# Kernel optimization log

Measured on AMD Instinct MI355X. Metric: run time of the kernel, lower is better.

The kernel has to match this reference:

```python
import jax, jax.numpy as jnp
import numpy as np

NU, NI, E, D, B, L = 100000, 50000, 800000, 64, 1024, 2
P_DROP, TEMP = 0.25, 0.2
L1, L2, L3 = 0.2, 0.01, 1e-5


def setup_inputs() -> dict:
    k = jax.random.split(jax.random.key(0), 20)
    s = 0.02  # xavier-ish scale for embedding tables
    return dict(
        E_u_0=jax.random.normal(k[0], (NU, D), jnp.float32) * s,
        E_i_0=jax.random.normal(k[1], (NI, D), jnp.float32) * s,
        fuse_w=jax.random.normal(k[2], (E,), jnp.float32),
        fuse_b=jax.random.normal(k[3], (E,), jnp.float32),
        W1u=jax.random.normal(k[4], (D, D), jnp.float32) / np.sqrt(D),
        W1i=jax.random.normal(k[5], (D, D), jnp.float32) / np.sqrt(D),
        b1=jnp.zeros((D,), jnp.float32),
        W2=jax.random.normal(k[6], (D,), jnp.float32) / np.sqrt(D),
        b2=jnp.zeros((1,), jnp.float32),
        att_a=jax.random.normal(k[7], (2 * D,), jnp.float32) / np.sqrt(2 * D),
        wv_param=jax.random.normal(k[8], (E,), jnp.float32),
        Wg=jax.random.normal(k[9], (D, D), jnp.float32) / np.sqrt(D),
        adj_vals=jax.random.uniform(k[10], (E,), jnp.float32, 0.001, 0.02),
        drop_main_u=jax.random.uniform(k[11], (2 * L, E), jnp.float32),
        drop_aug_u=jax.random.uniform(k[12], (2 * L, E), jnp.float32),
        edge_src=jax.random.randint(k[13], (E,), 0, NU),
        edge_dst=jax.random.randint(k[14], (E,), 0, NI),
        uids=jax.random.randint(k[15], (B,), 0, NU),
        iids=jax.random.randint(k[16], (B,), 0, NI),
        pos_ids=jax.random.randint(k[17], (B,), 0, NI),
        neg_ids=jax.random.randint(k[18], (B,), 0, NI),
    )


def _forward(E_u_0, E_i_0, fuse_w, fuse_b, W1u, W1i, b1, W2, b2, att_a,
             wv_param, Wg, adj_vals, drop_main_u, drop_aug_u,
             edge_src, edge_dst, uids, iids, pos_ids, neg_ids):
    dt = adj_vals.dtype

    def spmm_u(vals, Xi):  # A @ Xi -> [NU, D]
        return jax.ops.segment_sum(vals[:, None] * Xi[edge_dst], edge_src, num_segments=NU)

    def spmm_i(vals, Xu):  # A.T @ Xu -> [NI, D]
        return jax.ops.segment_sum(vals[:, None] * Xu[edge_src], edge_dst, num_segments=NI)

    def mask(u):  # sparse_dropout: keep w.p. 1-p, rescale
        return (u > P_DROP).astype(dt) / (1.0 - P_DROP)

    def propagate(vals, drops):  # LightGCN-style sum over layers
        Eu, Ei = E_u_0, E_i_0
        Su, Si = Eu, Ei
        for layer in range(L):
            Eu_n = spmm_u(vals * mask(drops[2 * layer]), Ei)
            Ei_n = spmm_i(vals * mask(drops[2 * layer + 1]), Eu)
            Eu, Ei = Eu_n, Ei_n
            Su, Si = Su + Eu, Si + Ei
        return Su, Si

    E_u, E_i = propagate(adj_vals, drop_main_u)

    eu0, ei0 = E_u_0[edge_src], E_i_0[edge_dst]  # [E, D]
    # MLP view
    h = jax.nn.relu(eu0 @ W1u + ei0 @ W1i + b1)
    Ag_mlp = jax.nn.sigmoid(h @ W2 + b2[0])
    # WV view: learnable per-edge weight
    Ag_wv = jax.nn.sigmoid(wv_param)
    # GCN view: one propagation on current embeddings, bilinear edge score
    h_u = spmm_u(adj_vals, E_i)
    h_i = spmm_i(adj_vals, E_u)
    Ag_gcn = jax.nn.sigmoid(jnp.sum((h_u[edge_src] @ Wg) * h_i[edge_dst], axis=1))
    # ATT view: GAT-style
    Ag_att = jax.nn.sigmoid(jax.nn.leaky_relu(eu0 @ att_a[:D] + ei0 @ att_a[D:], 0.2))

    views = jnp.stack([Ag_mlp, Ag_wv, Ag_gcn, Ag_att])  # [4, E]
    w = jax.nn.softmax(jnp.tanh(fuse_w * views + fuse_b), axis=1)  # softmax over edges (as in source)
    Ag = jnp.sum(w * views, axis=0)
    Ag = (Ag + (views - Ag).sum(0)) / 5.0  # mlp_cof = 1 -> (sum(views) - 3*Ag) / 5

    # refine: sigmoid of endpoint dot products
    pre = jax.nn.sigmoid(jnp.sum(E_u[edge_src] * E_i[edge_dst], axis=1))
    baew = pre * Ag  # batch_aug_edge_weight

    aug_vals = jax.lax.stop_gradient(baew) * adj_vals  # new_graph * adj_norm (detach + Hadamard)
    Z_u, Z_i = propagate(aug_vals, drop_aug_u)

    # contrastive loss
    Gu, Gi = Z_u[uids], Z_i[iids]
    neg_sc = jnp.log(jnp.exp(Gu @ E_u.T / TEMP).sum(1) + 1e-8).mean() \
           + jnp.log(jnp.exp(Gi @ E_i.T / TEMP).sum(1) + 1e-8).mean()
    pos_sc = jnp.clip((Gu * E_u[uids]).sum(1) / TEMP, -5.0, 5.0).mean() \
           + jnp.clip((Gi * E_i[iids]).sum(1) / TEMP, -5.0, 5.0).mean()
    loss_cl = -pos_sc + neg_sc

    # BPR loss
    u_e, p_e, n_e = E_u[uids], E_i[pos_ids], E_i[neg_ids]
    diff = (u_e * p_e).sum(-1) - (u_e * n_e).sum(-1)
    loss_bpr = -jnp.log(jax.nn.sigmoid(diff)).mean()

    loss_pr = L2 * (-jnp.log(baew)).mean()

    params = [E_u_0, E_i_0, fuse_w, fuse_b, W1u, W1i, b1, W2, b2, att_a, wv_param, Wg]
    loss_reg = L3 * sum((p_ ** 2).sum() for p_ in params)

    loss = loss_bpr + L1 * loss_cl + loss_pr + loss_reg
    return loss, loss_bpr, L1 * loss_cl, loss_pr


def reference(E_u_0, E_i_0, fuse_w, fuse_b, W1u, W1i, b1, W2, b2, att_a,
              wv_param, Wg, adj_vals, drop_main_u, drop_aug_u,
              edge_src, edge_dst, uids, iids, pos_ids, neg_ids):
    return _forward(E_u_0, E_i_0, fuse_w, fuse_b, W1u, W1i, b1, W2, b2, att_a,
                    wv_param, Wg, adj_vals, drop_main_u, drop_aug_u,
                    edge_src, edge_dst, uids, iids, pos_ids, neg_ids)
```

## Files before the change

kernel.cpp:

```cpp
#include <hip/hip_runtime.h>
#include <math.h>

constexpr int NUc = 100000;
constexpr int NIc = 50000;
constexpr int Ec  = 800000;
constexpr int Bc  = 1024;

typedef __attribute__((ext_vector_type(8))) short short8;
typedef __attribute__((ext_vector_type(8))) unsigned short ushort8;
typedef __attribute__((ext_vector_type(4))) unsigned short ushort4v;
typedef __attribute__((ext_vector_type(4))) float floatx4;

__device__ __forceinline__ float sigf(float x) { return 1.f / (1.f + __expf(-x)); }
__device__ __forceinline__ float maskf(float u) { return (u > 0.25f) ? (1.f / 0.75f) : 0.f; }
__device__ __forceinline__ unsigned short f2bf(float f) {
    unsigned int u = __float_as_uint(f);
    unsigned int r = (u + 0x7fffu + ((u >> 16) & 1u)) >> 16;
    return (unsigned short)r;
}
__device__ __forceinline__ float bf2f(unsigned short u) {
    return __uint_as_float((unsigned int)u << 16);
}

__global__ void hist_both(const int* __restrict__ esrc, const int* __restrict__ edst,
                          int* __restrict__ cntAll, int n) {
    int i = blockIdx.x * blockDim.x + threadIdx.x;
    if (i < n) {
        atomicAdd(&cntAll[esrc[i]], 1);
        atomicAdd(&cntAll[NUc + edst[i]], 1);
    }
}

__global__ void scan_block(const int* __restrict__ cnt, int* __restrict__ scanAll,
                           int* __restrict__ bsum, int N) {
    __shared__ int sh[1024];
    int i = blockIdx.x * 1024 + threadIdx.x;
    int v = (i < N) ? cnt[i] : 0;
    sh[threadIdx.x] = v;
    __syncthreads();
    for (int off = 1; off < 1024; off <<= 1) {
        int t = (threadIdx.x >= off) ? sh[threadIdx.x - off] : 0;
        __syncthreads();
        sh[threadIdx.x] += t;
        __syncthreads();
    }
    if (i < N) scanAll[i] = sh[threadIdx.x];
    if (threadIdx.x == 1023) bsum[blockIdx.x] = sh[1023];
}

__global__ void scan_bsums(int* __restrict__ bsum, int nb) {
    __shared__ int sh[256];
    int t = threadIdx.x;
    int v = (t < nb) ? bsum[t] : 0;
    sh[t] = v;
    __syncthreads();
    for (int off = 1; off < 256; off <<= 1) {
        int x = (t >= off) ? sh[t - off] : 0;
        __syncthreads();
        sh[t] += x;
        __syncthreads();
    }
    if (t < nb) bsum[t] = sh[t] - v;
}

__global__ void scan_add_cur(const int* __restrict__ scanAll, const int* __restrict__ bsum,
                             const int* __restrict__ cnt,
                             int* __restrict__ rpu, int* __restrict__ rpi,
                             int* __restrict__ curu, int* __restrict__ curi) {
    int i = blockIdx.x * blockDim.x + threadIdx.x;
    if (i >= NUc + NIc) return;
    int v = scanAll[i] + bsum[i >> 10];
    if (i < NUc) {
        rpu[i + 1] = v;
        if (i == 0) rpu[0] = 0;
        curu[i] = v - cnt[i];
    } else {
        int j = i - NUc;
        rpi[j + 1] = v - Ec;
        if (j == 0) rpi[0] = 0;
        curi[j] = v - Ec - cnt[i];
    }
}

__global__ void fill_both(const int* __restrict__ esrc, const int* __restrict__ edst,
                          int* __restrict__ curu, int* __restrict__ curi,
                          int* __restrict__ colu, int* __restrict__ posu, int* __restrict__ permu,
                          int* __restrict__ coli, int* __restrict__ permi, int n) {
    int i = blockIdx.x * blockDim.x + threadIdx.x;
    if (i >= n) return;
    int s = esrc[i], d = edst[i];
    int pu = atomicAdd(&curu[s], 1);
    colu[pu] = d; posu[i] = pu; permu[pu] = i;
    int pi = atomicAdd(&curi[d], 1);
    coli[pi] = s; permi[pi] = i;
}

__global__ void build_rowu(const int* __restrict__ rp, int* __restrict__ rowu, int N) {
    int r = blockIdx.x * blockDim.x + threadIdx.x;
    if (r < N) {
        int s = rp[r], e = rp[r + 1];
        for (int p = s; p < e; ++p) rowu[p] = r;
    }
}

__global__ void build_w_main_both(const int* __restrict__ permu, const int* __restrict__ permi,
                                  const float* __restrict__ adj, const float* __restrict__ dmain,
                                  float* __restrict__ wMu0, float* __restrict__ wMu1,
                                  float* __restrict__ adjPu,
                                  float* __restrict__ wMi0, float* __restrict__ wMi1,
                                  float* __restrict__ adjPi) {
    int p = blockIdx.x * blockDim.x + threadIdx.x;
    if (p < Ec) {
        int e = permu[p];
        float a = adj[e];
        wMu0[p] = a * maskf(dmain[e]);
        wMu1[p] = a * maskf(dmain[2 * (size_t)Ec + e]);
        adjPu[p] = a;
    } else if (p < 2 * Ec) {
        p -= Ec;
        int e = permi[p];
        float a = adj[e];
        wMi0[p] = a * maskf(dmain[(size_t)Ec + e]);
        wMi1[p] = a * maskf(dmain[3 * (size_t)Ec + e]);
        adjPi[p] = a;
    }
}

__global__ void build_w_aug_both(const int* __restrict__ permu, const int* __restrict__ permi,
                                 const float* __restrict__ av, const float* __restrict__ daug,
                                 float* __restrict__ wAu0, float* __restrict__ wAu1,
                                 float* __restrict__ wAi0, float* __restrict__ wAi1) {
    int p = blockIdx.x * blockDim.x + threadIdx.x;
    if (p < Ec) {
        int e = permu[p];
        float a = av[e];
        wAu0[p] = a * maskf(daug[e]);
        wAu1[p] = a * maskf(daug[2 * (size_t)Ec + e]);
    } else if (p < 2 * Ec) {
        p -= Ec;
        int e = permi[p];
        float a = av[e];
        wAi0[p] = a * maskf(daug[(size_t)Ec + e]);
        wAi1[p] = a * maskf(daug[3 * (size_t)Ec + e]);
    }
}

__device__ __forceinline__ void spmm_core(
        const int* __restrict__ rp, const int* __restrict__ col,
        const float* __restrict__ w, const unsigned short* __restrict__ Xbf,
        float* __restrict__ Acc, const float* __restrict__ Base,
        unsigned short* __restrict__ Ybf, unsigned short* __restrict__ Accbf,
        int row, int lane) {
    int s = rp[row], e = rp[row + 1];
    float acc = 0.f;
    int j = s;
    for (; j + 4 <= e; j += 4) {
        int c0 = col[j], c1 = col[j + 1], c2 = col[j + 2], c3 = col[j + 3];
        float w0 = w[j], w1 = w[j + 1], w2 = w[j + 2], w3 = w[j + 3];
        float x0 = bf2f(Xbf[(size_t)c0 * 64 + lane]);
        float x1 = bf2f(Xbf[(size_t)c1 * 64 + lane]);
        float x2 = bf2f(Xbf[(size_t)c2 * 64 + lane]);
        float x3 = bf2f(Xbf[(size_t)c3 * 64 + lane]);
        acc = fmaf(w0, x0, acc);
        acc = fmaf(w1, x1, acc);
        acc = fmaf(w2, x2, acc);
        acc = fmaf(w3, x3, acc);
    }
    for (; j < e; ++j) acc = fmaf(w[j], bf2f(Xbf[(size_t)col[j] * 64 + lane]), acc);
    size_t o = (size_t)row * 64 + lane;
    if (Acc) {
        float nv = (Base ? Base[o] : Acc[o]) + acc;
        Acc[o] = nv;
        if (Accbf) Accbf[o] = f2bf(nv);
    }
    if (Ybf) Ybf[o] = f2bf(acc);
}

__global__ void spmm_bf2(int blocksA,
        const int* __restrict__ rpA, const int* __restrict__ colA, const float* __restrict__ wA,
        const unsigned short* __restrict__ XA, float* __restrict__ AccA,
        const float* __restrict__ BaseA, unsigned short* __restrict__ YA,
        unsigned short* __restrict__ AbfA, int NA,
        const int* __restrict__ rpB, const int* __restrict__ colB, const float* __restrict__ wB,
        const unsigned short* __restrict__ XB, float* __restrict__ AccB,
        const float* __restrict__ BaseB, unsigned short* __restrict__ YB,
        unsigned short* __restrict__ AbfB, int NB) {
    int lane = threadIdx.x & 63;
    int w4 = threadIdx.x >> 6;
    int bx = blockIdx.x;
    if (bx < blocksA) {
        int row = bx * 4 + w4;
        if (row < NA) spmm_core(rpA, colA, wA, XA, AccA, BaseA, YA, AbfA, row, lane);
    } else {
        int row = (bx - blocksA) * 4 + w4;
        if (row < NB) spmm_core(rpB, colB, wB, XB, AccB, BaseB, YB, AbfB, row, lane);
    }
}

__global__ void prep_PU(const unsigned short* __restrict__ Eu0bf,
                        const unsigned short* __restrict__ hubf,
                        const unsigned short* __restrict__ Subf,
                        const float* __restrict__ W1, const float* __restrict__ Wg,
                        const float* __restrict__ att,
                        unsigned short* __restrict__ PU, float* __restrict__ auv, int N) {
    __shared__ float W1l[4096];
    __shared__ float Wgl[4096];
    for (int i = threadIdx.x; i < 4096; i += blockDim.x) { W1l[i] = W1[i]; Wgl[i] = Wg[i]; }
    __syncthreads();
    int wid = blockIdx.x * (blockDim.x >> 6) + (threadIdx.x >> 6);
    int lane = threadIdx.x & 63;
    for (int r = 0; r < 8; ++r) {
        int row = wid * 8 + r;
        if (row >= N) break;
        const unsigned short* xr = Eu0bf + (size_t)row * 64;
        const unsigned short* hr = hubf + (size_t)row * 64;
        float a1 = 0.f, a2 = 0.f, ad = 0.f;
#pragma unroll
        for (int k = 0; k < 64; ++k) {
            float xv = bf2f(xr[k]);
            a1 = fmaf(xv, W1l[k * 64 + lane], a1);
            a2 = fmaf(bf2f(hr[k]), Wgl[k * 64 + lane], a2);
            ad = fmaf(xv, att[k], ad);
        }
        size_t base = (size_t)row * 192;
        PU[base + lane]       = f2bf(a1);
        PU[base + 64 + lane]  = f2bf(a2);
        PU[base + 128 + lane] = Subf[(size_t)row * 64 + lane];
        if (lane == 0) auv[row] = ad;
    }
}

__global__ void prep_PI(const unsigned short* __restrict__ Ei0bf,
                        const unsigned short* __restrict__ hibf,
                        const unsigned short* __restrict__ Sibf,
                        const float* __restrict__ W1, const float* __restrict__ att,
                        unsigned short* __restrict__ PI, float* __restrict__ aiv, int N) {
    __shared__ float W1l[4096];
    for (int i = threadIdx.x; i < 4096; i += blockDim.x) W1l[i] = W1[i];
    __syncthreads();
    int wid = blockIdx.x * (blockDim.x >> 6) + (threadIdx.x >> 6);
    int lane = threadIdx.x & 63;
    for (int r = 0; r < 8; ++r) {
        int row = wid * 8 + r;
        if (row >= N) break;
        const unsigned short* xr = Ei0bf + (size_t)row * 64;
        float a1 = 0.f, ad = 0.f;
#pragma unroll
        for (int k = 0; k < 64; ++k) {
            float xv = bf2f(xr[k]);
            a1 = fmaf(xv, W1l[k * 64 + lane], a1);
            ad = fmaf(xv, att[k], ad);
        }
        size_t base = (size_t)row * 192;
        PI[base + lane]       = f2bf(a1);
        PI[base + 64 + lane]  = hibf[(size_t)row * 64 + lane];
        PI[base + 128 + lane] = Sibf[(size_t)row * 64 + lane];
        if (lane == 0) aiv[row] = ad;
    }
}

__global__ void cvt_both(const float4* __restrict__ Xu, ushort4* __restrict__ Yu, int n4u,
                         const float4* __restrict__ Xi, ushort4* __restrict__ Yi, int n4i) {
    int i = blockIdx.x * blockDim.x + threadIdx.x;
    if (i < n4u) {
        float4 v = Xu[i];
        Yu[i] = make_ushort4(f2bf(v.x), f2bf(v.y), f2bf(v.z), f2bf(v.w));
    } else {
        i -= n4u;
        if (i < n4i) {
            float4 v = Xi[i];
            Yi[i] = make_ushort4(f2bf(v.x), f2bf(v.y), f2bf(v.z), f2bf(v.w));
        }
    }
}

__global__ void __launch_bounds__(128) edge_pass1(
        const int* __restrict__ rowu, const int* __restrict__ colP,
        const unsigned short* __restrict__ PU, const unsigned short* __restrict__ PI,
        const float* __restrict__ b1, const float* __restrict__ W2,
        const float* __restrict__ b2,
        const float* __restrict__ auv, const float* __restrict__ aiv,
        float4* __restrict__ vp4, int E) {
    __shared__ ushort4v lds4[128 * 49];
    int p0 = blockIdx.x * 128;
    int tid = threadIdx.x;
#pragma unroll
    for (int it = 0; it < 24; ++it) {
        int flat = it * 128 + tid;
        int row = flat / 24, c = flat - row * 24;
        int d = colP[p0 + row];
        ushort8 g = *(const ushort8*)(PI + (size_t)d * 192 + c * 8);
        ushort4v lo = {g[0], g[1], g[2], g[3]};
        ushort4v hi = {g[4], g[5], g[6], g[7]};
        lds4[row * 49 + c * 2]     = lo;
        lds4[row * 49 + c * 2 + 1] = hi;
    }
    __syncthreads();
    int p = p0 + tid;
    int s = rowu[p];
    int d = colP[p];
    const ushort8* pu = (const ushort8*)(PU + (size_t)s * 192);
    const ushort4v* pl = lds4 + tid * 49;
    float r1 = 0.f, r2 = 0.f, r3 = 0.f;
#pragma unroll
    for (int k = 0; k < 8; ++k) {
        ushort8 u1 = pu[k], hu = pu[8 + k], su = pu[16 + k];
        ushort4v i1a = pl[2 * k], i1b = pl[2 * k + 1];
        ushort4v hia = pl[16 + 2 * k], hib = pl[16 + 2 * k + 1];
        ushort4v sia = pl[32 + 2 * k], sib = pl[32 + 2 * k + 1];
#pragma unroll
        for (int j = 0; j < 4; ++j) {
            float h = bf2f(u1[j]) + bf2f(i1a[j]) + b1[k * 8 + j];
            r1 = fmaf(fmaxf(h, 0.f), W2[k * 8 + j], r1);
            r2 = fmaf(bf2f(hu[j]), bf2f(hia[j]), r2);
            r3 = fmaf(bf2f(su[j]), bf2f(sia[j]), r3);
        }
#pragma unroll
        for (int j = 0; j < 4; ++j) {
            float h = bf2f(u1[4 + j]) + bf2f(i1b[j]) + b1[k * 8 + 4 + j];
            r1 = fmaf(fmaxf(h, 0.f), W2[k * 8 + 4 + j], r1);
            r2 = fmaf(bf2f(hu[4 + j]), bf2f(hib[j]), r2);
            r3 = fmaf(bf2f(su[4 + j]), bf2f(sib[j]), r3);
        }
    }
    float v0 = sigf(r1 + b2[0]);
    float v2 = sigf(r2);
    float ax = auv[s] + aiv[d];
    float v3 = sigf(ax > 0.f ? ax : 0.2f * ax);
    float pre = sigf(r3);
    vp4[p] = make_float4(v0, v2, v3, pre);
}

__global__ void edge_pass2a(const float4* __restrict__ vp4, const int* __restrict__ posu,
                            const float* __restrict__ fw, const float* __restrict__ fb,
                            const float* __restrict__ wv,
                            float4* __restrict__ viewsE, float* __restrict__ preE,
                            float* __restrict__ sumexp, int E) {
    int e = blockIdx.x * blockDim.x + threadIdx.x;
    float ex0 = 0.f, ex1 = 0.f, ex2 = 0.f, ex3 = 0.f;
    if (e < E) {
        float4 t = vp4[posu[e]];
        float v0 = t.x, v2 = t.y, v3 = t.z;
        float v1 = sigf(wv[e]);
        viewsE[e] = make_float4(v0, v1, v2, v3);
        preE[e] = t.w;
        float fwe = fw[e], fbe = fb[e];
        ex0 = __expf(tanhf(fmaf(fwe, v0, fbe)));
        ex1 = __expf(tanhf(fmaf(fwe, v1, fbe)));
        ex2 = __expf(tanhf(fmaf(fwe, v2, fbe)));
        ex3 = __expf(tanhf(fmaf(fwe, v3, fbe)));
    }
#pragma unroll
    for (int off = 32; off; off >>= 1) {
        ex0 += __shfl_xor(ex0, off, 64);
        ex1 += __shfl_xor(ex1, off, 64);
        ex2 += __shfl_xor(ex2, off, 64);
        ex3 += __shfl_xor(ex3, off, 64);
    }
    __shared__ float sh[4][4];
    int w = threadIdx.x >> 6;
    if ((threadIdx.x & 63) == 0) {
        sh[w][0] = ex0; sh[w][1] = ex1; sh[w][2] = ex2; sh[w][3] = ex3;
    }
    __syncthreads();
    if (threadIdx.x < 4)
        atomicAdd(&sumexp[threadIdx.x],
                  sh[0][threadIdx.x] + sh[1][threadIdx.x] + sh[2][threadIdx.x] + sh[3][threadIdx.x]);
}

__global__ void edge_pass2b(const float4* __restrict__ viewsE, const float* __restrict__ preE,
                            const float* __restrict__ fw, const float* __restrict__ fb,
                            const float* __restrict__ adj, const float* __restrict__ sumexp,
                            float* __restrict__ av, float* __restrict__ neglog, int E) {
    int e = blockIdx.x * blockDim.x + threadIdx.x;
    float nl = 0.f;
    if (e < E) {
        float s0 = sumexp[0], s1 = sumexp[1], s2 = sumexp[2], s3 = sumexp[3];
        float4 v = viewsE[e];
        float fwe = fw[e], fbe = fb[e];
        float w0 = __expf(tanhf(fmaf(fwe, v.x, fbe))) / s0;
        float w1 = __expf(tanhf(fmaf(fwe, v.y, fbe))) / s1;
        float w2 = __expf(tanhf(fmaf(fwe, v.z, fbe))) / s2;
        float w3 = __expf(tanhf(fmaf(fwe, v.w, fbe))) / s3;
        float agw = w0 * v.x + w1 * v.y + w2 * v.z + w3 * v.w;
        float sv = v.x + v.y + v.z + v.w;
        float Ag = (sv - 3.f * agw) * 0.2f;
        float bw = preE[e] * Ag;
        av[e] = bw * adj[e];
        nl = -logf(bw);
    }
#pragma unroll
    for (int off = 32; off; off >>= 1) nl += __shfl_xor(nl, off, 64);
    __shared__ float sh4[4];
    if ((threadIdx.x & 63) == 0) sh4[threadIdx.x >> 6] = nl;
    __syncthreads();
    if (threadIdx.x == 0) atomicAdd(neglog, sh4[0] + sh4[1] + sh4[2] + sh4[3]);
}

__global__ void gather_cvt_both(const float* __restrict__ Zu, const int* __restrict__ uids,
                                unsigned short* __restrict__ Gu,
                                const float* __restrict__ Zi, const int* __restrict__ iids,
                                unsigned short* __restrict__ Gi) {
    int t = blockIdx.x * blockDim.x + threadIdx.x;
    if (t < Bc * 64) {
        Gu[t] = f2bf(Zu[(size_t)uids[t >> 6] * 64 + (t & 63)]);
    } else {
        t -= Bc * 64;
        if (t < Bc * 64) Gi[t] = f2bf(Zi[(size_t)iids[t >> 6] * 64 + (t & 63)]);
    }
}

__device__ __forceinline__ void lse_core(const unsigned short* __restrict__ Gbf,
                                         const unsigned short* __restrict__ Ebf,
                                         float* __restrict__ sums, int N, int tilesPerChunk,
                                         int wid, int lane) {
    int bgroup = wid & 15;
    int chunk = wid >> 4;
    int ntiles = N >> 4;
    int t0 = chunk * tilesPerChunk;
    if (t0 >= ntiles) return;
    int t1 = t0 + tilesPerChunk; if (t1 > ntiles) t1 = ntiles;
    int m = lane & 15, quad = lane >> 4;

    short8 a0[4], a1[4];
#pragma unroll
    for (int t = 0; t < 4; ++t) {
        const short8* ap = (const short8*)(Gbf + ((size_t)(bgroup * 64 + t * 16 + m)) * 64 + quad * 8);
        a0[t] = ap[0];
        a1[t] = ap[4];
    }
    floatx4 rs[4];
#pragma unroll
    for (int t = 0; t < 4; ++t) rs[t] = (floatx4){0.f, 0.f, 0.f, 0.f};

    for (int jt = t0; jt < t1; ++jt) {
        const short8* bp = (const short8*)(Ebf + ((size_t)(jt * 16 + m)) * 64 + quad * 8);
        short8 bf0 = bp[0], bf1 = bp[4];
#pragma unroll
        for (int t = 0; t < 4; ++t) {
            floatx4 c = (floatx4){0.f, 0.f, 0.f, 0.f};
            c = __builtin_amdgcn_mfma_f32_16x16x32_bf16(a0[t], bf0, c, 0, 0, 0);
            c = __builtin_amdgcn_mfma_f32_16x16x32_bf16(a1[t], bf1, c, 0, 0, 0);
#pragma unroll
            for (int r = 0; r < 4; ++r) rs[t][r] += __expf(c[r] * 5.f);
        }
    }
#pragma unroll
    for (int t = 0; t < 4; ++t) {
#pragma unroll
        for (int r = 0; r < 4; ++r) {
            float v = rs[t][r];
            v += __shfl_xor(v, 1, 64);
            v += __shfl_xor(v, 2, 64);
            v += __shfl_xor(v, 4, 64);
            v += __shfl_xor(v, 8, 64);
            if (m == 0) atomicAdd(&sums[bgroup * 64 + t * 16 + quad * 4 + r], v);
        }
    }
}

__global__ void lse_both(const unsigned short* __restrict__ Gu, const unsigned short* __restrict__ Su,
                         float* __restrict__ sums_u,
                         const unsigned short* __restrict__ Gi, const unsigned short* __restrict__ Si,
                         float* __restrict__ sums_i) {
    int lane = threadIdx.x & 63;
    int w4 = threadIdx.x >> 6;
    if ((int)blockIdx.x < 640) {
        lse_core(Gu, Su, sums_u, NUc, 40, blockIdx.x * 4 + w4, lane);
    } else {
        lse_core(Gi, Si, sums_i, NIc, 40, (blockIdx.x - 640) * 4 + w4, lane);
    }
}

__global__ void batch_partial(const float* __restrict__ Su, const float* __restrict__ Si,
                              const float* __restrict__ Zu, const float* __restrict__ Zi,
                              const int* __restrict__ uids, const int* __restrict__ iids,
                              const int* __restrict__ pids, const int* __restrict__ nids,
                              float* __restrict__ pos_b, float* __restrict__ bpr_b) {
    int b = blockIdx.x * (blockDim.x >> 6) + (threadIdx.x >> 6);
    if (b >= Bc) return;
    int lane = threadIdx.x & 63;
    int u = uids[b], ii = iids[b], p = pids[b], n = nids[b];
    float zu = Zu[(size_t)u * 64 + lane],  su = Su[(size_t)u * 64 + lane];
    float zi = Zi[(size_t)ii * 64 + lane], si = Si[(size_t)ii * 64 + lane];
    float pe = Si[(size_t)p * 64 + lane],  ne = Si[(size_t)n * 64 + lane];
    float du = zu * su, di = zi * si, dp = su * pe, dn = su * ne;
#pragma unroll
    for (int off = 32; off; off >>= 1) {
        du += __shfl_xor(du, off, 64);
        di += __shfl_xor(di, off, 64);
        dp += __shfl_xor(dp, off, 64);
        dn += __shfl_xor(dn, off, 64);
    }
    if (lane == 0) {
        pos_b[b] = fminf(fmaxf(du * 5.f, -5.f), 5.f) + fminf(fmaxf(di * 5.f, -5.f), 5.f);
        bpr_b[b] = log1pf(__expf(-(dp - dn)));
    }
}

__global__ void sumsq_all(const float* __restrict__ p0, const float* __restrict__ p1,
                          const float* __restrict__ p2, const float* __restrict__ p3,
                          const float* __restrict__ p4, const float* __restrict__ p5,
                          const float* __restrict__ p6, const float* __restrict__ p7,
                          const float* __restrict__ p8, const float* __restrict__ p9,
                          const float* __restrict__ p10, const float* __restrict__ p11,
                          float* __restrict__ acc) {
    const int TOT = 6400000 + 3200000 + 3 * 800000 + 3 * 4096 + 128 + 64 + 64 + 1;
    float s = 0.f;
    for (int t = blockIdx.x * blockDim.x + threadIdx.x; t < TOT; t += gridDim.x * blockDim.x) {
        int i = t;
        const float* P;
        if (i < 6400000) P = p0;
        else if ((i -= 6400000) < 3200000) P = p1;
        else if ((i -= 3200000) < 800000) P = p2;
        else if ((i -= 800000) < 800000) P = p3;
        else if ((i -= 800000) < 800000) P = p4;
        else if ((i -= 800000) < 4096) P = p5;
        else if ((i -= 4096) < 4096) P = p6;
        else if ((i -= 4096) < 4096) P = p7;
        else if ((i -= 4096) < 128) P = p8;
        else if ((i -= 128) < 64) P = p9;
        else if ((i -= 64) < 64) P = p10;
        else { i -= 64; P = p11; }
        float v = P[i];
        s = fmaf(v, v, s);
    }
#pragma unroll
    for (int off = 32; off; off >>= 1) s += __shfl_xor(s, off, 64);
    __shared__ float sh[4];
    if ((threadIdx.x & 63) == 0) sh[threadIdx.x >> 6] = s;
    __syncthreads();
    if (threadIdx.x == 0) atomicAdd(acc, sh[0] + sh[1] + sh[2] + sh[3]);
}

__global__ void finalize_kernel(const float* __restrict__ sumexp_u, const float* __restrict__ sumexp_i,
                                const float* __restrict__ pos_b, const float* __restrict__ bpr_b,
                                const float* __restrict__ neglog, const float* __restrict__ regsum,
                                float* __restrict__ out) {
    int b = threadIdx.x;
    float lse = logf(sumexp_u[b] + 1e-8f) + logf(sumexp_i[b] + 1e-8f);
    float pos = pos_b[b];
    float bpr = bpr_b[b];
#pragma unroll
    for (int off = 32; off; off >>= 1) {
        lse += __shfl_xor(lse, off, 64);
        pos += __shfl_xor(pos, off, 64);
        bpr += __shfl_xor(bpr, off, 64);
    }
    __shared__ float sl[16], sp[16], sb[16];
    int w = b >> 6;
    if ((b & 63) == 0) { sl[w] = lse; sp[w] = pos; sb[w] = bpr; }
    __syncthreads();
    if (b == 0) {
        float L = 0.f, P = 0.f, Bz = 0.f;
        for (int i = 0; i < 16; ++i) { L += sl[i]; P += sp[i]; Bz += sb[i]; }
        float neg_sc = L * (1.f / Bc);
        float pos_sc = P * (1.f / Bc);
        float loss_cl = neg_sc - pos_sc;
        float l1cl = 0.2f * loss_cl;
        float loss_bpr = Bz * (1.f / Bc);
        float loss_pr = 0.01f * (neglog[0] * (1.f / Ec));
        float loss_reg = 1e-5f * regsum[0];
        out[0] = loss_bpr + l1cl + loss_pr + loss_reg;
        out[1] = loss_bpr;
        out[2] = l1cl;
        out[3] = loss_pr;
    }
}

extern "C" void kernel_launch(void* const* d_in, const int* in_sizes, int n_in,
                              void* d_out, int out_size, void* d_ws, size_t ws_size,
                              hipStream_t stream) {
    const float* Eu0    = (const float*)d_in[0];
    const float* Ei0    = (const float*)d_in[1];
    const float* fuse_w = (const float*)d_in[2];
    const float* fuse_b = (const float*)d_in[3];
    const float* W1u    = (const float*)d_in[4];
    const float* W1i    = (const float*)d_in[5];
    const float* b1     = (const float*)d_in[6];
    const float* W2     = (const float*)d_in[7];
    const float* b2     = (const float*)d_in[8];
    const float* att    = (const float*)d_in[9];
    const float* wv     = (const float*)d_in[10];
    const float* Wg     = (const float*)d_in[11];
    const float* adj    = (const float*)d_in[12];
    const float* dmain  = (const float*)d_in[13];
    const float* daug   = (const float*)d_in[14];
    const int*   esrc   = (const int*)d_in[15];
    const int*   edst   = (const int*)d_in[16];
    const int*   uids   = (const int*)d_in[17];
    const int*   iids   = (const int*)d_in[18];
    const int*   pids   = (const int*)d_in[19];
    const int*   nids   = (const int*)d_in[20];
    float* out = (float*)d_out;

    char* base = (char*)d_ws;
    size_t off = 0;
    auto alloc = [&](size_t bytes) -> char* {
        char* pp = base + off;
        off = (off + bytes + 255) & ~(size_t)255;
        return pp;
    };
    float* Su   = (float*)alloc((size_t)NUc * 64 * 4);
    float* Si   = (float*)alloc((size_t)NIc * 64 * 4);
    char* blkZ = alloc((size_t)NUc * 64 * 4 + (size_t)NIc * 64 * 4);
    unsigned short* PU = (unsigned short*)blkZ;
    float4* viewsE = (float4*)blkZ;
    float* preE   = (float*)(blkZ + (size_t)Ec * 16);
    float* Zu = (float*)blkZ;
    float* Zi = (float*)(blkZ + (size_t)NUc * 64 * 4);
    float4* vp4 = (float4*)alloc((size_t)Ec * 16);
    unsigned short* Eu0bf = (unsigned short*)alloc((size_t)NUc * 64 * 2);
    unsigned short* Ei0bf = (unsigned short*)alloc((size_t)NIc * 64 * 2);
    unsigned short* Subf  = (unsigned short*)alloc((size_t)NUc * 64 * 2);
    unsigned short* Sibf  = (unsigned short*)alloc((size_t)NIc * 64 * 2);
    unsigned short* Bubf  = (unsigned short*)alloc((size_t)NUc * 64 * 2);
    unsigned short* Bibf  = (unsigned short*)alloc((size_t)NIc * 64 * 2);
    unsigned short* hubf  = (unsigned short*)alloc((size_t)NUc * 64 * 2);
    unsigned short* hibf  = (unsigned short*)alloc((size_t)NIc * 64 * 2);
    char* blkA = alloc((size_t)Ec * 4 * 6);
    float* adjPu = (float*)blkA;
    float* adjPi = (float*)(blkA + (size_t)Ec * 4);
    float* wAu0  = (float*)(blkA + (size_t)Ec * 8);
    float* wAu1  = (float*)(blkA + (size_t)Ec * 12);
    float* wAi0  = (float*)(blkA + (size_t)Ec * 16);
    float* wAi1  = (float*)(blkA + (size_t)Ec * 20);
    unsigned short* PI = (unsigned short*)blkA;
    float* wMu0  = (float*)alloc((size_t)Ec * 4);
    float* wMu1  = (float*)alloc((size_t)Ec * 4);
    float* wMi0  = (float*)alloc((size_t)Ec * 4);
    float* wMi1  = (float*)alloc((size_t)Ec * 4);
    float* av    = (float*)alloc((size_t)Ec * 4);
    float* auv  = (float*)alloc((size_t)NUc * 4);
    float* aiv  = (float*)alloc((size_t)NIc * 4);
    int* rowu  = (int*)alloc((size_t)Ec * 4);
    unsigned short* Gubf = (unsigned short*)alloc((size_t)Bc * 64 * 2);
    unsigned short* Gibf = (unsigned short*)alloc((size_t)Bc * 64 * 2);
    float* scal = (float*)alloc((4 + 1 + 1 + 2 + Bc + Bc) * 4);
    float* sumexp4 = scal;
    float* neglog  = scal + 4;
    float* regsum  = scal + 5;
    float* sumexp_u = scal + 8;
    float* sumexp_i = scal + 8 + Bc;
    float* pos_b = (float*)alloc((size_t)Bc * 4);
    float* bpr_b = (float*)alloc((size_t)Bc * 4);
    int* rpu   = (int*)alloc((size_t)(NUc + 1) * 4);
    int* rpi   = (int*)alloc((size_t)(NIc + 1) * 4);
    int* colu  = (int*)alloc((size_t)Ec * 4);
    int* coli  = (int*)alloc((size_t)Ec * 4);
    int* posu  = (int*)alloc((size_t)Ec * 4);
    int* permu = (int*)alloc((size_t)Ec * 4);
    int* permi = (int*)alloc((size_t)Ec * 4);
    int* cntAll  = (int*)alloc((size_t)(NUc + NIc) * 4);
    int* scanAll = (int*)alloc((size_t)(NUc + NIc) * 4);
    int* curu  = (int*)alloc((size_t)NUc * 4);
    int* curi  = (int*)alloc((size_t)NIc * 4);
    int* bsum  = (int*)alloc(256 * 4);

    dim3 b256(256);
    const int NALL = NUc + NIc;
    const int nbAll = (NALL + 1023) / 1024;
    const dim3 gE((Ec + 255) / 256);
    const dim3 g2E((2 * Ec + 255) / 256);
    const int blocksU = (NUc + 3) / 4, blocksI = (NIc + 3) / 4;
    const dim3 gUI(blocksU + blocksI);
    const dim3 gU8((NUc + 31) / 32), gI8((NIc + 31) / 32);

    hipMemsetAsync(cntAll, 0, (size_t)NALL * 4, stream);
    hipMemsetAsync(scal, 0, (4 + 1 + 1 + 2 + Bc + Bc) * 4, stream);

    hist_both<<<gE, b256, 0, stream>>>(esrc, edst, cntAll, Ec);
    scan_block<<<dim3(nbAll), dim3(1024), 0, stream>>>(cntAll, scanAll, bsum, NALL);
    scan_bsums<<<dim3(1), dim3(256), 0, stream>>>(bsum, nbAll);
    scan_add_cur<<<dim3((NALL + 255) / 256), b256, 0, stream>>>(scanAll, bsum, cntAll,
                                                               rpu, rpi, curu, curi);
    fill_both<<<gE, b256, 0, stream>>>(esrc, edst, curu, curi, colu, posu, permu, coli, permi, Ec);
    build_rowu<<<dim3((NUc + 255) / 256), b256, 0, stream>>>(rpu, rowu, NUc);

    build_w_main_both<<<g2E, b256, 0, stream>>>(permu, permi, adj, dmain,
                                                wMu0, wMu1, adjPu, wMi0, wMi1, adjPi);

    cvt_both<<<dim3(((NUc + NIc) * 16 + 255) / 256), b256, 0, stream>>>(
        (const float4*)Eu0, (ushort4*)Eu0bf, NUc * 16,
        (const float4*)Ei0, (ushort4*)Ei0bf, NIc * 16);

    spmm_bf2<<<gUI, b256, 0, stream>>>(blocksU,
        rpu, colu, wMu0, Ei0bf, Su, Eu0, Bubf, nullptr, NUc,
        rpi, coli, wMi0, Eu0bf, Si, Ei0, Bibf, nullptr, NIc);
    spmm_bf2<<<gUI, b256, 0, stream>>>(blocksU,
        rpu, colu, wMu1, Bibf, Su, nullptr, nullptr, Subf, NUc,
        rpi, coli, wMi1, Bubf, Si, nullptr, nullptr, Sibf, NIc);

    spmm_bf2<<<gUI, b256, 0, stream>>>(blocksU,
        rpu, colu, adjPu, Sibf, nullptr, nullptr, hubf, nullptr, NUc,
        rpi, coli, adjPi, Subf, nullptr, nullptr, hibf, nullptr, NIc);

    prep_PU<<<gU8, b256, 0, stream>>>(Eu0bf, hubf, Subf, W1u, Wg, att, PU, auv, NUc);
    prep_PI<<<gI8, b256, 0, stream>>>(Ei0bf, hibf, Sibf, W1i, att + 64, PI, aiv, NIc);

    edge_pass1<<<dim3(Ec / 128), dim3(128), 0, stream>>>(
        rowu, colu, PU, PI, b1, W2, b2, auv, aiv, vp4, Ec);

    edge_pass2a<<<gE, b256, 0, stream>>>(vp4, posu, fuse_w, fuse_b, wv,
                                         viewsE, preE, sumexp4, Ec);

    edge_pass2b<<<gE, b256, 0, stream>>>(
        viewsE, preE, fuse_w, fuse_b, adj, sumexp4, av, neglog, Ec);

    build_w_aug_both<<<g2E, b256, 0, stream>>>(permu, permi, av, daug, wAu0, wAu1, wAi0, wAi1);

    spmm_bf2<<<gUI, b256, 0, stream>>>(blocksU,
        rpu, colu, wAu0, Ei0bf, Zu, Eu0, Bubf, nullptr, NUc,
        rpi, coli, wAi0, Eu0bf, Zi, Ei0, Bibf, nullptr, NIc);
    spmm_bf2<<<gUI, b256, 0, stream>>>(blocksU,
        rpu, colu, wAu1, Bibf, Zu, nullptr, nullptr, nullptr, NUc,
        rpi, coli, wAi1, Bubf, Zi, nullptr, nullptr, nullptr, NIc);

    gather_cvt_both<<<dim3((2 * Bc * 64 + 255) / 256), b256, 0, stream>>>(
        Zu, uids, Gubf, Zi, iids, Gibf);
    lse_both<<<dim3(960), b256, 0, stream>>>(Gubf, Subf, sumexp_u, Gibf, Sibf, sumexp_i);

    batch_partial<<<dim3(Bc / 4), b256, 0, stream>>>(Su, Si, Zu, Zi, uids, iids, pids, nids,
                                                     pos_b, bpr_b);

    sumsq_all<<<dim3(4096), b256, 0, stream>>>(Eu0, Ei0, fuse_w, fuse_b, wv,
                                               W1u, W1i, Wg, att, b1, W2, b2, regsum);

    finalize_kernel<<<dim3(1), dim3(1024), 0, stream>>>(
        sumexp_u, sumexp_i, pos_b, bpr_b, neglog, regsum, out);
}
```

Before: 1.253 ms.

## Merge user/item projection prep kernels and compute them with bf16 MFMA

```diff
diff --git a/kernel.cpp b/kernel.cpp
--- a/kernel.cpp
+++ b/kernel.cpp
@@ -197,65 +197,104 @@
     }
 }
 
-__global__ void prep_PU(const unsigned short* __restrict__ Eu0bf,
-                        const unsigned short* __restrict__ hubf,
-                        const unsigned short* __restrict__ Subf,
-                        const float* __restrict__ W1, const float* __restrict__ Wg,
-                        const float* __restrict__ att,
-                        unsigned short* __restrict__ PU, float* __restrict__ auv, int N) {
-    __shared__ float W1l[4096];
-    __shared__ float Wgl[4096];
-    for (int i = threadIdx.x; i < 4096; i += blockDim.x) { W1l[i] = W1[i]; Wgl[i] = Wg[i]; }
+constexpr int WT = 68;
+__global__ void __launch_bounds__(256) prep_both(
+        const unsigned short* __restrict__ Eu0bf, const unsigned short* __restrict__ hubf,
+        const unsigned short* __restrict__ Subf,
+        const unsigned short* __restrict__ Ei0bf, const unsigned short* __restrict__ hibf,
+        const unsigned short* __restrict__ Sibf,
+        const float* __restrict__ W1u, const float* __restrict__ Wg,
+        const float* __restrict__ W1i, const float* __restrict__ att,
+        unsigned short* __restrict__ PU, unsigned short* __restrict__ PI,
+        float* __restrict__ auv, float* __restrict__ aiv, int blocksU) {
+    __shared__ unsigned short WtA[64 * WT];
+    __shared__ unsigned short WtB[64 * WT];
+    bool uside = (int)blockIdx.x < blocksU;
+    const float* Wa = uside ? W1u : W1i;
+    for (int t = threadIdx.x; t < 4096; t += 256) {
+        int n = t >> 6, k = t & 63;
+        WtA[n * WT + k] = f2bf(Wa[k * 64 + n]);
+        if (uside) WtB[n * WT + k] = f2bf(Wg[k * 64 + n]);
+    }
     __syncthreads();
-    int wid = blockIdx.x * (blockDim.x >> 6) + (threadIdx.x >> 6);
+
     int lane = threadIdx.x & 63;
-    for (int r = 0; r < 8; ++r) {
-        int row = wid * 8 + r;
-        if (row >= N) break;
-        const unsigned short* xr = Eu0bf + (size_t)row * 64;
-        const unsigned short* hr = hubf + (size_t)row * 64;
-        float a1 = 0.f, a2 = 0.f, ad = 0.f;
-#pragma unroll
-        for (int k = 0; k < 64; ++k) {
-            float xv = bf2f(xr[k]);
-            a1 = fmaf(xv, W1l[k * 64 + lane], a1);
-            a2 = fmaf(bf2f(hr[k]), Wgl[k * 64 + lane], a2);
-            ad = fmaf(xv, att[k], ad);
+    int m = lane & 15, quad = lane >> 4;
+    int wv = threadIdx.x >> 6;
+
+    int tile, ntiles;
+    const unsigned short* X;
+    unsigned short* P;
+    const float* attp;
+    float* aout;
+    if (uside) {
+        tile = blockIdx.x * 4 + wv; ntiles = NUc / 16;
+        X = Eu0bf; P = PU; attp = att; aout = auv;
+    } else {
+        tile = (blockIdx.x - blocksU) * 4 + wv; ntiles = NIc / 16;
+        X = Ei0bf; P = PI; attp = att + 64; aout = aiv;
+    }
+    if (tile >= ntiles) return;
+    int row0 = tile * 16;
+
+    short8 bA[4][2], bB[4][2];
+#pragma unroll
+    for (int tt = 0; tt < 4; ++tt) {
+#pragma unroll
+        for (int kf = 0; kf < 2; ++kf) {
+            bA[tt][kf] = *(const short8*)(WtA + (tt * 16 + m) * WT + kf * 32 + quad * 8);
+            if (uside) bB[tt][kf] = *(const short8*)(WtB + (tt * 16 + m) * WT + kf * 32 + quad * 8);
         }
-        size_t base = (size_t)row * 192;
-        PU[base + lane]       = f2bf(a1);
-        PU[base + 64 + lane]  = f2bf(a2);
-        PU[base + 128 + lane] = Subf[(size_t)row * 64 + lane];
-        if (lane == 0) auv[row] = ad;
-    }
-}
-
-__global__ void prep_PI(const unsigned short* __restrict__ Ei0bf,
-                        const unsigned short* __restrict__ hibf,
-                        const unsigned short* __restrict__ Sibf,
-                        const float* __restrict__ W1, const float* __restrict__ att,
-                        unsigned short* __restrict__ PI, float* __restrict__ aiv, int N) {
-    __shared__ float W1l[4096];
-    for (int i = threadIdx.x; i < 4096; i += blockDim.x) W1l[i] = W1[i];
-    __syncthreads();
-    int wid = blockIdx.x * (blockDim.x >> 6) + (threadIdx.x >> 6);
-    int lane = threadIdx.x & 63;
-    for (int r = 0; r < 8; ++r) {
-        int row = wid * 8 + r;
-        if (row >= N) break;
-        const unsigned short* xr = Ei0bf + (size_t)row * 64;
-        float a1 = 0.f, ad = 0.f;
-#pragma unroll
-        for (int k = 0; k < 64; ++k) {
-            float xv = bf2f(xr[k]);
-            a1 = fmaf(xv, W1l[k * 64 + lane], a1);
-            ad = fmaf(xv, att[k], ad);
+    }
+    const short8* ap = (const short8*)(X + (size_t)(row0 + m) * 64 + quad * 8);
+    short8 a0 = ap[0], a1 = ap[4];
+
+#pragma unroll
+    for (int tt = 0; tt < 4; ++tt) {
+        floatx4 c = (floatx4){0.f, 0.f, 0.f, 0.f};
+        c = __builtin_amdgcn_mfma_f32_16x16x32_bf16(a0, bA[tt][0], c, 0, 0, 0);
+        c = __builtin_amdgcn_mfma_f32_16x16x32_bf16(a1, bA[tt][1], c, 0, 0, 0);
+#pragma unroll
+        for (int r = 0; r < 4; ++r)
+            P[(size_t)(row0 + quad * 4 + r) * 192 + tt * 16 + m] = f2bf(c[r]);
+    }
+    if (uside) {
+        const short8* hp = (const short8*)(hubf + (size_t)(row0 + m) * 64 + quad * 8);
+        short8 h0 = hp[0], h1 = hp[4];
+#pragma unroll
+        for (int tt = 0; tt < 4; ++tt) {
+            floatx4 c = (floatx4){0.f, 0.f, 0.f, 0.f};
+            c = __builtin_amdgcn_mfma_f32_16x16x32_bf16(h0, bB[tt][0], c, 0, 0, 0);
+            c = __builtin_amdgcn_mfma_f32_16x16x32_bf16(h1, bB[tt][1], c, 0, 0, 0);
+#pragma unroll
+            for (int r = 0; r < 4; ++r)
+                P[(size_t)(row0 + quad * 4 + r) * 192 + 64 + tt * 16 + m] = f2bf(c[r]);
         }
-        size_t base = (size_t)row * 192;
-        PI[base + lane]       = f2bf(a1);
-        PI[base + 64 + lane]  = hibf[(size_t)row * 64 + lane];
-        PI[base + 128 + lane] = Sibf[(size_t)row * 64 + lane];
-        if (lane == 0) aiv[row] = ad;
+    } else {
+#pragma unroll
+        for (int t = 0; t < 2; ++t) {
+            int c = lane * 2 + t;
+            int row = c >> 3, o8 = (c & 7) * 8;
+            *(ushort8*)(P + (size_t)(row0 + row) * 192 + 64 + o8) =
+                *(const ushort8*)(hibf + (size_t)(row0 + row) * 64 + o8);
+        }
+    }
+    const unsigned short* Sb = uside ? Subf : Sibf;
+#pragma unroll
+    for (int t = 0; t < 2; ++t) {
+        int c = lane * 2 + t;
+        int row = c >> 3, o8 = (c & 7) * 8;
+        *(ushort8*)(P + (size_t)(row0 + row) * 192 + 128 + o8) =
+            *(const ushort8*)(Sb + (size_t)(row0 + row) * 64 + o8);
+    }
+    {
+        const unsigned short* xr = X + (size_t)(row0 + m) * 64 + quad * 16;
+        float ad = 0.f;
+#pragma unroll
+        for (int j = 0; j < 16; ++j) ad = fmaf(bf2f(xr[j]), attp[quad * 16 + j], ad);
+        ad += __shfl_xor(ad, 16, 64);
+        ad += __shfl_xor(ad, 32, 64);
+        if (lane < 16) aout[row0 + lane] = ad;
     }
 }
 
@@ -664,7 +703,6 @@
     const dim3 g2E((2 * Ec + 255) / 256);
     const int blocksU = (NUc + 3) / 4, blocksI = (NIc + 3) / 4;
     const dim3 gUI(blocksU + blocksI);
-    const dim3 gU8((NUc + 31) / 32), gI8((NIc + 31) / 32);
 
     hipMemsetAsync(cntAll, 0, (size_t)NALL * 4, stream);
     hipMemsetAsync(scal, 0, (4 + 1 + 1 + 2 + Bc + Bc) * 4, stream);
@@ -695,8 +733,13 @@
         rpu, colu, adjPu, Sibf, nullptr, nullptr, hubf, nullptr, NUc,
         rpi, coli, adjPi, Subf, nullptr, nullptr, hibf, nullptr, NIc);
 
-    prep_PU<<<gU8, b256, 0, stream>>>(Eu0bf, hubf, Subf, W1u, Wg, att, PU, auv, NUc);
-    prep_PI<<<gI8, b256, 0, stream>>>(Ei0bf, hibf, Sibf, W1i, att + 64, PI, aiv, NIc);
+    {
+        const int tBU = (NUc / 16 + 3) / 4;
+        const int tBI = (NIc / 16 + 3) / 4;
+        prep_both<<<dim3(tBU + tBI), b256, 0, stream>>>(
+            Eu0bf, hubf, Subf, Ei0bf, hibf, Sibf,
+            W1u, Wg, W1i, att, PU, PI, auv, aiv, tBU);
+    }
 
     edge_pass1<<<dim3(Ec / 128), dim3(128), 0, stream>>>(
         rowu, colu, PU, PI, b1, W2, b2, auv, aiv, vp4, Ec);
```

After: 1.164 ms. 1.08x faster.
